# Kernel optimization log

Hardware: AMD Instinct MI355X
Metric: run time of the kernel (lower is better)

## Reference

```python
import jax, jax.numpy as jnp
import numpy as np

B, T, IN, H, NL = 64, 256, 64, 768, 2
LU, OUT = 256, 1
INPUT_SCALE = 1.5
OUTPUT_SCALE = 70.0
STD = 0.001  # nn.init.normal_(p, std=0.001) on all LSTM params


def setup_inputs() -> dict:
    key = jax.random.key(0)
    ks = jax.random.split(key, 16)
    inp = {"x": jax.random.normal(ks[0], (B, T, IN), jnp.float32)}
    dims = [IN, H]
    for l in range(NL):
        d = dims[l]
        inp[f"Wih{l}"] = (jax.random.normal(ks[1 + 4 * l], (4 * H, d)) * STD).astype(jnp.float32)
        inp[f"Whh{l}"] = (jax.random.normal(ks[2 + 4 * l], (4 * H, H)) * STD).astype(jnp.float32)
        inp[f"bih{l}"] = (jax.random.normal(ks[3 + 4 * l], (4 * H,)) * STD).astype(jnp.float32)
        inp[f"bhh{l}"] = (jax.random.normal(ks[4 + 4 * l], (4 * H,)) * STD).astype(jnp.float32)
    # MLP head (torch default-ish small init)
    inp["W1"] = (jax.random.normal(ks[9], (LU, H)) * (1.0 / np.sqrt(H))).astype(jnp.float32)
    inp["b1"] = jnp.zeros((LU,), jnp.float32)
    inp["W2"] = (jax.random.normal(ks[10], (OUT, LU)) * (1.0 / np.sqrt(LU))).astype(jnp.float32)
    inp["b2"] = jnp.zeros((OUT,), jnp.float32)
    return inp


def _lstm_layer(x, Wih, Whh, bih, bhh):
    # x: (B, T, D) -> hidden sequence (B, T, H). PyTorch gate order: i, f, g, o.
    b = x.shape[0]
    h = Whh.shape[1]
    # precompute input contributions for all timesteps: (B, T, 4H)
    xg = jnp.einsum('btd,gd->btg', x, Wih) + bih + bhh

    def step(carry, xt):
        hp, cp = carry
        gates = xt + hp @ Whh.T  # (B, 4H)
        i, f, g, o = jnp.split(gates, 4, axis=-1)
        c = jax.nn.sigmoid(f) * cp + jax.nn.sigmoid(i) * jnp.tanh(g)
        hn = jax.nn.sigmoid(o) * jnp.tanh(c)
        return (hn, c), hn

    h0 = jnp.zeros((b, h), x.dtype)
    (_, _), hs = jax.lax.scan(step, (h0, h0), xg.transpose(1, 0, 2))
    return hs.transpose(1, 0, 2)  # (B, T, H)


def reference(x, Wih0, Whh0, bih0, bhh0, Wih1, Whh1, bih1, bhh1, W1, b1, W2, b2):
    xs = x / INPUT_SCALE
    h1 = _lstm_layer(xs, Wih0, Whh0, bih0, bhh0)
    h2 = _lstm_layer(h1, Wih1, Whh1, bih1, bhh1)
    last = h2[:, -1, :]                       # (B, H)
    z = jax.nn.soft_sign(last @ W1.T + b1)    # Softsign: x / (1 + |x|)
    pred = (z @ W2.T + b2) * OUTPUT_SCALE     # (B, OUT)
    return pred[:, None, :]                   # unsqueeze(1) -> (B, 1, OUT)
```

## Files before the change

kernel.cpp:

```cpp
#include <hip/hip_runtime.h>
#include <hip/hip_bf16.h>


#define B_  64
#define T_  256
#define IN_ 64
#define H_  768
#define G_  3072
#define K0_ 832
#define K1_ 1536
#define NWG0 96
#define NWG  192
#define CB_  96
#define SLOT_ (CB_ * 64 * 8)

typedef __bf16 bf16_t;
typedef bf16_t bf16x8 __attribute__((ext_vector_type(8)));
typedef float  f32x4  __attribute__((ext_vector_type(4)));

__device__ __forceinline__ unsigned short f2bf(float f) {
    union { float f; unsigned u; } v; v.f = f;
    unsigned r = v.u + 0x7FFFu + ((v.u >> 16) & 1u);
    return (unsigned short)(r >> 16);
}
__device__ __forceinline__ float sigm(float x) {
    return 1.0f / (1.0f + expf(-x));
}
__device__ __forceinline__ void st_llc_u32(unsigned* p, unsigned v) {
    asm volatile("global_store_dword %0, %1, off sc1" :: "v"(p), "v"(v) : "memory");
}
#define MFMA16(a, b, c) __builtin_amdgcn_mfma_f32_16x16x32_bf16((a), (b), (c), 0, 0, 0)

__global__ __launch_bounds__(256) void prep_kernel(
    const float* __restrict__ x,
    const float* __restrict__ Wih0, const float* __restrict__ Whh0,
    const float* __restrict__ bih0, const float* __restrict__ bhh0,
    const float* __restrict__ Wih1, const float* __restrict__ Whh1,
    const float* __restrict__ bih1, const float* __restrict__ bhh1,
    unsigned short* __restrict__ xsT,
    unsigned short* __restrict__ W0cat,
    unsigned short* __restrict__ W1cat,
    float* __restrict__ bias0, float* __restrict__ bias1,
    int* __restrict__ flags)
{
    int i = blockIdx.x * blockDim.x + threadIdx.x;
    int stride = gridDim.x * blockDim.x;
    for (int j = i; j < B_ * T_ * IN_; j += stride) {
        int b = j >> 14;
        int t = (j >> 6) & (T_ - 1);
        int k = j & (IN_ - 1);
        xsT[(((size_t)t * B_) + b) * IN_ + k] = f2bf(x[j] * (1.0f / 1.5f));
    }
    for (int j = i; j < G_ * IN_; j += stride) {
        int r = j >> 6; int k = j & 63;
        W0cat[(size_t)r * K0_ + k] = f2bf(Wih0[j]);
    }
    for (int j = i; j < G_ * H_; j += stride) {
        int r = j / H_; int k = j - r * H_;
        W0cat[(size_t)r * K0_ + IN_ + k] = f2bf(Whh0[j]);
        W1cat[(size_t)r * K1_ + k]       = f2bf(Wih1[j]);
        W1cat[(size_t)r * K1_ + H_ + k]  = f2bf(Whh1[j]);
    }
    for (int j = i; j < G_; j += stride) {
        bias0[j] = bih0[j] + bhh0[j];
        bias1[j] = bih1[j] + bhh1[j];
    }
    for (int j = i; j < 256; j += stride)
        flags[j] = ((j & 127) < NWG0) ? 0 : 0x7FFFFFFF;
}

__global__ __launch_bounds__(256) void lstm_persistent(
    const unsigned short* __restrict__ xsT,
    const unsigned short* __restrict__ W0cat,
    const unsigned short* __restrict__ W1cat,
    const float* __restrict__ bias0, const float* __restrict__ bias1,
    unsigned short* __restrict__ h1ring,
    unsigned short* __restrict__ h2ring,
    float* __restrict__ hf32,
    int* __restrict__ flags)
{
    __shared__ unsigned short ldsb[4][16][8];

    const int tid  = threadIdx.x;
    const int lane = tid & 63;
    const int wave = tid >> 6;
    const int wg   = blockIdx.x;
    const bool isL1 = (wg >= NWG0);
    const int cb   = isL1 ? (wg - NWG0) : wg;
    const int c0   = cb * 8;
    const int frow = lane & 15;
    const int q    = lane >> 4;
    const int kof  = q * 8;
    const int m0   = wave * 16;

    int* flags0 = &flags[0];
    int* flags1 = &flags[128];
    const int pi1 = lane;
    const int pi2 = 64 + (lane & 31);

    const unsigned short* Wc = isL1 ? W1cat : W0cat;
    const int Kc = isL1 ? K1_ : K0_;
    int q0 = frow >> 3,        col0 = c0 + (frow & 7);
    const unsigned short* Bp0 = Wc + (size_t)(q0 * H_ + col0) * Kc + kof;
    const unsigned short* Bp1 = Wc + (size_t)((2 + q0) * H_ + col0) * Kc + kof;

    const float* bias = isL1 ? bias1 : bias0;
    const bool lowhalf = (lane & 15) < 8;
    const int ecol = c0 + (lane & 7);
    float bi = 0.f, bff = 0.f, bg = 0.f, bo = 0.f;
    if (lowhalf) {
        bi  = bias[0 * H_ + ecol];
        bff = bias[1 * H_ + ecol];
        bg  = bias[2 * H_ + ecol];
        bo  = bias[3 * H_ + ecol];
    }
    float creg[4] = {0.f, 0.f, 0.f, 0.f};

    const size_t aoff = (size_t)q * 512 + (size_t)(m0 + frow) * 8;
    const size_t stoff_e = (size_t)cb * 512 + (size_t)(m0 + (lane >> 2)) * 8
                         + (size_t)(lane & 3) * 2;

    if (!isL1) {
        for (int s = 0; s < T_; ++s) {
            f32x4 acc0 = {0.f, 0.f, 0.f, 0.f};
            f32x4 acc1 = {0.f, 0.f, 0.f, 0.f};
            {
                const unsigned short* xsp =
                    xsT + ((size_t)s * B_ + m0 + frow) * IN_ + kof;
                #pragma unroll
                for (int ki = 0; ki < 2; ki++) {
                    bf16x8 a  = *(const bf16x8*)(xsp + ki * 32);
                    bf16x8 b0 = *(const bf16x8*)(Bp0 + ki * 32);
                    bf16x8 b1 = *(const bf16x8*)(Bp1 + ki * 32);
                    acc0 = MFMA16(a, b0, acc0);
                    acc1 = MFMA16(a, b1, acc1);
                }
            }
            if (s > 0) {
                if (wave == 0) {
                    for (;;) {
                        int fa = __hip_atomic_load(&flags0[pi1], __ATOMIC_RELAXED,
                                                   __HIP_MEMORY_SCOPE_AGENT);
                        int fb = __hip_atomic_load(&flags0[pi2], __ATOMIC_RELAXED,
                                                   __HIP_MEMORY_SCOPE_AGENT);
                        if (__all(fa >= s && fb >= s)) break;
                        __builtin_amdgcn_s_sleep(1);
                    }
                }
                __syncthreads();
                const unsigned short* hr = h1ring + (size_t)(s - 1) * SLOT_ + aoff;
                #pragma unroll
                for (int kj = 0; kj < 24; kj++) {
                    bf16x8 a  = *(const bf16x8*)(hr + kj * 2048);
                    bf16x8 b0 = *(const bf16x8*)(Bp0 + (kj + 2) * 32);
                    bf16x8 b1 = *(const bf16x8*)(Bp1 + (kj + 2) * 32);
                    acc0 = MFMA16(a, b0, acc0);
                    acc1 = MFMA16(a, b1, acc1);
                }
            }
            f32x4 pacc0, pacc1;
            #pragma unroll
            for (int j = 0; j < 4; j++) {
                pacc0[j] = __shfl_xor(acc0[j], 8);
                pacc1[j] = __shfl_xor(acc1[j], 8);
            }
            if (lowhalf) {
                #pragma unroll
                for (int j = 0; j < 4; j++) {
                    float pi = acc0[j]  + bi;
                    float pf = pacc0[j] + bff;
                    float pg = acc1[j]  + bg;
                    float po = pacc1[j] + bo;
                    float cn = sigm(pf) * creg[j] + sigm(pi) * tanhf(pg);
                    float hn = sigm(po) * tanhf(cn);
                    creg[j] = cn;
                    ldsb[wave][q * 4 + j][lane & 7] = f2bf(hn);
                }
            }
            unsigned v = ((const unsigned*)&ldsb[wave][0][0])[lane];
            st_llc_u32((unsigned*)(h1ring + (size_t)s * SLOT_ + stoff_e), v);
            __syncthreads();
            if (tid == 0) st_llc_u32((unsigned*)&flags0[cb], (unsigned)(s + 1));
        }
    } else {
        for (int s = 1; s <= T_; ++s) {
            const int t = s - 1;
            if (wave == 0) {
                for (;;) {
                    int fa = __hip_atomic_load(&flags0[pi1], __ATOMIC_RELAXED,
                                               __HIP_MEMORY_SCOPE_AGENT);
                    int fb = __hip_atomic_load(&flags0[pi2], __ATOMIC_RELAXED,
                                               __HIP_MEMORY_SCOPE_AGENT);
                    int ga = __hip_atomic_load(&flags1[pi1], __ATOMIC_RELAXED,
                                               __HIP_MEMORY_SCOPE_AGENT);
                    int gb = __hip_atomic_load(&flags1[pi2], __ATOMIC_RELAXED,
                                               __HIP_MEMORY_SCOPE_AGENT);
                    if (__all(fa >= s && fb >= s && ga >= s - 1 && gb >= s - 1))
                        break;
                    __builtin_amdgcn_s_sleep(1);
                }
            }
            __syncthreads();
            f32x4 acc0 = {0.f, 0.f, 0.f, 0.f};
            f32x4 acc1 = {0.f, 0.f, 0.f, 0.f};
            const unsigned short* h1r = h1ring + (size_t)t * SLOT_ + aoff;
            #pragma unroll
            for (int ki = 0; ki < 24; ki++) {
                bf16x8 a  = *(const bf16x8*)(h1r + ki * 2048);
                bf16x8 b0 = *(const bf16x8*)(Bp0 + ki * 32);
                bf16x8 b1 = *(const bf16x8*)(Bp1 + ki * 32);
                acc0 = MFMA16(a, b0, acc0);
                acc1 = MFMA16(a, b1, acc1);
            }
            if (t > 0) {
                const unsigned short* h2r = h2ring + (size_t)(t - 1) * SLOT_ + aoff;
                #pragma unroll
                for (int ki = 0; ki < 24; ki++) {
                    bf16x8 a  = *(const bf16x8*)(h2r + ki * 2048);
                    bf16x8 b0 = *(const bf16x8*)(Bp0 + (ki + 24) * 32);
                    bf16x8 b1 = *(const bf16x8*)(Bp1 + (ki + 24) * 32);
                    acc0 = MFMA16(a, b0, acc0);
                    acc1 = MFMA16(a, b1, acc1);
                }
            }
            f32x4 pacc0, pacc1;
            #pragma unroll
            for (int j = 0; j < 4; j++) {
                pacc0[j] = __shfl_xor(acc0[j], 8);
                pacc1[j] = __shfl_xor(acc1[j], 8);
            }
            if (lowhalf) {
                #pragma unroll
                for (int j = 0; j < 4; j++) {
                    int row = m0 + q * 4 + j;
                    float pi = acc0[j]  + bi;
                    float pf = pacc0[j] + bff;
                    float pg = acc1[j]  + bg;
                    float po = pacc1[j] + bo;
                    float cn = sigm(pf) * creg[j] + sigm(pi) * tanhf(pg);
                    float hn = sigm(po) * tanhf(cn);
                    creg[j] = cn;
                    ldsb[wave][q * 4 + j][lane & 7] = f2bf(hn);
                    if (t == T_ - 1) hf32[(size_t)row * H_ + ecol] = hn;
                }
            }
            unsigned v = ((const unsigned*)&ldsb[wave][0][0])[lane];
            st_llc_u32((unsigned*)(h2ring + (size_t)t * SLOT_ + stoff_e), v);
            __syncthreads();
            if (tid == 0) st_llc_u32((unsigned*)&flags1[cb], (unsigned)s);
        }
    }
}

__global__ __launch_bounds__(256) void head_kernel(
    const float* __restrict__ hlast,
    const float* __restrict__ W1, const float* __restrict__ b1,
    const float* __restrict__ W2, const float* __restrict__ b2,
    float* __restrict__ out)
{
    __shared__ float hs[H_];
    __shared__ float partial[4];
    int b = blockIdx.x;
    int tid = threadIdx.x;
    for (int j = tid; j < H_; j += 256) hs[j] = hlast[(size_t)b * H_ + j];
    __syncthreads();
    float z = 0.f;
    const float* w = W1 + (size_t)tid * H_;
    for (int j = 0; j < H_; j++) z += hs[j] * w[j];
    z += b1[tid];
    z = z / (1.0f + fabsf(z));
    float p = z * W2[tid];
    #pragma unroll
    for (int off = 32; off > 0; off >>= 1) p += __shfl_down(p, off, 64);
    if ((tid & 63) == 0) partial[tid >> 6] = p;
    __syncthreads();
    if (tid == 0) {
        float s = partial[0] + partial[1] + partial[2] + partial[3];
        out[b] = (s + b2[0]) * 70.0f;
    }
}

extern "C" void kernel_launch(void* const* d_in, const int* in_sizes, int n_in,
                              void* d_out, int out_size, void* d_ws, size_t ws_size,
                              hipStream_t stream) {
    const float* x    = (const float*)d_in[0];
    const float* Wih0 = (const float*)d_in[1];
    const float* Whh0 = (const float*)d_in[2];
    const float* bih0 = (const float*)d_in[3];
    const float* bhh0 = (const float*)d_in[4];
    const float* Wih1 = (const float*)d_in[5];
    const float* Whh1 = (const float*)d_in[6];
    const float* bih1 = (const float*)d_in[7];
    const float* bhh1 = (const float*)d_in[8];
    const float* W1   = (const float*)d_in[9];
    const float* b1   = (const float*)d_in[10];
    const float* W2   = (const float*)d_in[11];
    const float* b2   = (const float*)d_in[12];
    float* out = (float*)d_out;

    char* w = (char*)d_ws;
    int* flags = (int*)w;                         w += 2048;
    unsigned short* h1ring = (unsigned short*)w;  w += (size_t)T_ * SLOT_ * 2;
    unsigned short* h2ring = (unsigned short*)w;  w += (size_t)T_ * SLOT_ * 2;
    unsigned short* xsT    = (unsigned short*)w;  w += (size_t)B_ * T_ * IN_ * 2;
    unsigned short* W0cat  = (unsigned short*)w;  w += (size_t)G_ * K0_ * 2;
    unsigned short* W1cat  = (unsigned short*)w;  w += (size_t)G_ * K1_ * 2;
    float* bias0 = (float*)w;                     w += G_ * 4;
    float* bias1 = (float*)w;                     w += G_ * 4;
    float* hf32  = (float*)w;                     w += (size_t)B_ * H_ * 4;

    prep_kernel<<<1024, 256, 0, stream>>>(x, Wih0, Whh0, bih0, bhh0,
                                          Wih1, Whh1, bih1, bhh1,
                                          xsT, W0cat, W1cat, bias0, bias1, flags);
    lstm_persistent<<<NWG, 256, 0, stream>>>(xsT, W0cat, W1cat, bias0, bias1,
                                             h1ring, h2ring, hf32, flags);
    head_kernel<<<B_, 256, 0, stream>>>(hf32, W1, b1, W2, b2, out);
}
```

Measured before the change: 3.861 ms.

## Use per-wave flags for cross-block sync, fast activations, and spinning filler blocks

Replaces the block-wide barrier plus one-flag-per-workgroup handshake with per-wave flags. Each wave only waits on the same wave index of its producer blocks, since batch rows are independent, so waves progress decoupled without __syncthreads. Sigmoid and tanh are rewritten with hardware exp2/rcp intrinsics to cut the latency of the serial gate math, at some accuracy cost. The grid also gains 64 extra workgroups that spin on FMA loops until both layers finish, apparently to keep the device busy or clocked up. That adds power draw and may itself affect clocks.

```diff
diff --git a/kernel.cpp b/kernel.cpp
--- a/kernel.cpp
+++ b/kernel.cpp
@@ -10,9 +10,9 @@
 #define K0_ 832
 #define K1_ 1536
 #define NWG0 96
-#define NWG  192
-#define CB_  96
-#define SLOT_ (CB_ * 64 * 8)
+#define NWGC 192
+#define NWGT 256
+#define SLOT_ (96 * 64 * 8)
 
 typedef __bf16 bf16_t;
 typedef bf16_t bf16x8 __attribute__((ext_vector_type(8)));
@@ -23,13 +23,19 @@
     unsigned r = v.u + 0x7FFFu + ((v.u >> 16) & 1u);
     return (unsigned short)(r >> 16);
 }
-__device__ __forceinline__ float sigm(float x) {
-    return 1.0f / (1.0f + expf(-x));
+__device__ __forceinline__ float fast_sigm(float x) {
+    float e = __builtin_amdgcn_exp2f(-1.44269504f * x);
+    return __builtin_amdgcn_rcpf(1.0f + e);
+}
+__device__ __forceinline__ float fast_tanh(float x) {
+    float e = __builtin_amdgcn_exp2f(2.88539008f * x);
+    return (e - 1.0f) * __builtin_amdgcn_rcpf(e + 1.0f);
 }
 __device__ __forceinline__ void st_llc_u32(unsigned* p, unsigned v) {
     asm volatile("global_store_dword %0, %1, off sc1" :: "v"(p), "v"(v) : "memory");
 }
 #define MFMA16(a, b, c) __builtin_amdgcn_mfma_f32_16x16x32_bf16((a), (b), (c), 0, 0, 0)
+#define AGENT_LD(p) __hip_atomic_load((p), __ATOMIC_RELAXED, __HIP_MEMORY_SCOPE_AGENT)
 
 __global__ __launch_bounds__(256) void prep_kernel(
     const float* __restrict__ x,
@@ -65,7 +71,7 @@
         bias0[j] = bih0[j] + bhh0[j];
         bias1[j] = bih1[j] + bhh1[j];
     }
-    for (int j = i; j < 256; j += stride)
+    for (int j = i; j < 1024; j += stride)
         flags[j] = ((j & 127) < NWG0) ? 0 : 0x7FFFFFFF;
 }
 
@@ -85,6 +91,21 @@
     const int lane = tid & 63;
     const int wave = tid >> 6;
     const int wg   = blockIdx.x;
+
+    if (wg >= NWGC) {
+        float a = 1.0f + (float)wg * 1e-7f;
+        const float b = 1.0000001f, c = 1e-9f;
+        for (;;) {
+            #pragma unroll
+            for (int i = 0; i < 256; i++) a = __builtin_fmaf(a, b, c);
+            asm volatile("" : "+v"(a));
+            int f0 = AGENT_LD(&flags[0]);
+            int f1 = AGENT_LD(&flags[512]);
+            if (f0 >= T_ && f1 >= T_) break;
+        }
+        return;
+    }
+
     const bool isL1 = (wg >= NWG0);
     const int cb   = isL1 ? (wg - NWG0) : wg;
     const int c0   = cb * 8;
@@ -93,14 +114,14 @@
     const int kof  = q * 8;
     const int m0   = wave * 16;
 
-    int* flags0 = &flags[0];
-    int* flags1 = &flags[128];
-    const int pi1 = lane;
-    const int pi2 = 64 + (lane & 31);
+    int* fL0 = flags;
+    int* fL1 = flags + 512;
+    const int p1 = wave * 128 + lane;
+    const int p2 = wave * 128 + 64 + (lane & 31);
 
     const unsigned short* Wc = isL1 ? W1cat : W0cat;
     const int Kc = isL1 ? K1_ : K0_;
-    int q0 = frow >> 3,        col0 = c0 + (frow & 7);
+    int q0 = frow >> 3, col0 = c0 + (frow & 7);
     const unsigned short* Bp0 = Wc + (size_t)(q0 * H_ + col0) * Kc + kof;
     const unsigned short* Bp1 = Wc + (size_t)((2 + q0) * H_ + col0) * Kc + kof;
 
@@ -119,6 +140,8 @@
     const size_t aoff = (size_t)q * 512 + (size_t)(m0 + frow) * 8;
     const size_t stoff_e = (size_t)cb * 512 + (size_t)(m0 + (lane >> 2)) * 8
                          + (size_t)(lane & 3) * 2;
+    int* myflag0 = &fL0[wave * 128 + cb];
+    int* myflag1 = &fL1[wave * 128 + cb];
 
     if (!isL1) {
         for (int s = 0; s < T_; ++s) {
@@ -137,17 +160,13 @@
                 }
             }
             if (s > 0) {
-                if (wave == 0) {
-                    for (;;) {
-                        int fa = __hip_atomic_load(&flags0[pi1], __ATOMIC_RELAXED,
-                                                   __HIP_MEMORY_SCOPE_AGENT);
-                        int fb = __hip_atomic_load(&flags0[pi2], __ATOMIC_RELAXED,
-                                                   __HIP_MEMORY_SCOPE_AGENT);
-                        if (__all(fa >= s && fb >= s)) break;
-                        __builtin_amdgcn_s_sleep(1);
-                    }
-                }
-                __syncthreads();
+                for (;;) {
+                    int fa = AGENT_LD(&fL0[p1]);
+                    int fb = AGENT_LD(&fL0[p2]);
+                    if (__all(fa >= s && fb >= s)) break;
+                    __builtin_amdgcn_s_sleep(1);
+                }
+                asm volatile("" ::: "memory");
                 const unsigned short* hr = h1ring + (size_t)(s - 1) * SLOT_ + aoff;
                 #pragma unroll
                 for (int kj = 0; kj < 24; kj++) {
@@ -171,36 +190,30 @@
                     float pf = pacc0[j] + bff;
                     float pg = acc1[j]  + bg;
                     float po = pacc1[j] + bo;
-                    float cn = sigm(pf) * creg[j] + sigm(pi) * tanhf(pg);
-                    float hn = sigm(po) * tanhf(cn);
+                    float cn = fast_sigm(pf) * creg[j] + fast_sigm(pi) * fast_tanh(pg);
+                    float hn = fast_sigm(po) * fast_tanh(cn);
                     creg[j] = cn;
                     ldsb[wave][q * 4 + j][lane & 7] = f2bf(hn);
                 }
             }
             unsigned v = ((const unsigned*)&ldsb[wave][0][0])[lane];
             st_llc_u32((unsigned*)(h1ring + (size_t)s * SLOT_ + stoff_e), v);
-            __syncthreads();
-            if (tid == 0) st_llc_u32((unsigned*)&flags0[cb], (unsigned)(s + 1));
+            asm volatile("s_waitcnt vmcnt(0)" ::: "memory");
+            if (lane == 0) st_llc_u32((unsigned*)myflag0, (unsigned)(s + 1));
         }
     } else {
         for (int s = 1; s <= T_; ++s) {
             const int t = s - 1;
-            if (wave == 0) {
-                for (;;) {
-                    int fa = __hip_atomic_load(&flags0[pi1], __ATOMIC_RELAXED,
-                                               __HIP_MEMORY_SCOPE_AGENT);
-                    int fb = __hip_atomic_load(&flags0[pi2], __ATOMIC_RELAXED,
-                                               __HIP_MEMORY_SCOPE_AGENT);
-                    int ga = __hip_atomic_load(&flags1[pi1], __ATOMIC_RELAXED,
-                                               __HIP_MEMORY_SCOPE_AGENT);
-                    int gb = __hip_atomic_load(&flags1[pi2], __ATOMIC_RELAXED,
-                                               __HIP_MEMORY_SCOPE_AGENT);
-                    if (__all(fa >= s && fb >= s && ga >= s - 1 && gb >= s - 1))
-                        break;
-                    __builtin_amdgcn_s_sleep(1);
-                }
-            }
-            __syncthreads();
+            for (;;) {
+                int fa = AGENT_LD(&fL0[p1]);
+                int fb = AGENT_LD(&fL0[p2]);
+                int ga = AGENT_LD(&fL1[p1]);
+                int gb = AGENT_LD(&fL1[p2]);
+                if (__all(fa >= s && fb >= s && ga >= s - 1 && gb >= s - 1))
+                    break;
+                __builtin_amdgcn_s_sleep(1);
+            }
+            asm volatile("" ::: "memory");
             f32x4 acc0 = {0.f, 0.f, 0.f, 0.f};
             f32x4 acc1 = {0.f, 0.f, 0.f, 0.f};
             const unsigned short* h1r = h1ring + (size_t)t * SLOT_ + aoff;
@@ -232,22 +245,22 @@
             if (lowhalf) {
                 #pragma unroll
                 for (int j = 0; j < 4; j++) {
-                    int row = m0 + q * 4 + j;
                     float pi = acc0[j]  + bi;
                     float pf = pacc0[j] + bff;
                     float pg = acc1[j]  + bg;
                     float po = pacc1[j] + bo;
-                    float cn = sigm(pf) * creg[j] + sigm(pi) * tanhf(pg);
-                    float hn = sigm(po) * tanhf(cn);
+                    float cn = fast_sigm(pf) * creg[j] + fast_sigm(pi) * fast_tanh(pg);
+                    float hn = fast_sigm(po) * fast_tanh(cn);
                     creg[j] = cn;
                     ldsb[wave][q * 4 + j][lane & 7] = f2bf(hn);
-                    if (t == T_ - 1) hf32[(size_t)row * H_ + ecol] = hn;
+                    if (t == T_ - 1)
+                        hf32[(size_t)(m0 + q * 4 + j) * H_ + ecol] = hn;
                 }
             }
             unsigned v = ((const unsigned*)&ldsb[wave][0][0])[lane];
             st_llc_u32((unsigned*)(h2ring + (size_t)t * SLOT_ + stoff_e), v);
-            __syncthreads();
-            if (tid == 0) st_llc_u32((unsigned*)&flags1[cb], (unsigned)s);
+            asm volatile("s_waitcnt vmcnt(0)" ::: "memory");
+            if (lane == 0) st_llc_u32((unsigned*)myflag1, (unsigned)s);
         }
     }
 }
@@ -299,7 +312,7 @@
     float* out = (float*)d_out;
 
     char* w = (char*)d_ws;
-    int* flags = (int*)w;                         w += 2048;
+    int* flags = (int*)w;                         w += 4096;
     unsigned short* h1ring = (unsigned short*)w;  w += (size_t)T_ * SLOT_ * 2;
     unsigned short* h2ring = (unsigned short*)w;  w += (size_t)T_ * SLOT_ * 2;
     unsigned short* xsT    = (unsigned short*)w;  w += (size_t)B_ * T_ * IN_ * 2;
@@ -312,7 +325,7 @@
     prep_kernel<<<1024, 256, 0, stream>>>(x, Wih0, Whh0, bih0, bhh0,
                                           Wih1, Whh1, bih1, bhh1,
                                           xsT, W0cat, W1cat, bias0, bias1, flags);
-    lstm_persistent<<<NWG, 256, 0, stream>>>(xsT, W0cat, W1cat, bias0, bias1,
-                                             h1ring, h2ring, hf32, flags);
+    lstm_persistent<<<NWGT, 256, 0, stream>>>(xsT, W0cat, W1cat, bias0, bias1,
+                                              h1ring, h2ring, hf32, flags);
     head_kernel<<<B_, 256, 0, stream>>>(hf32, W1, b1, W2, b2, out);
 }
```

Result: slower. 6.314 ms (+63.5%).
